# Kernel tuning notes

Measured on AMD Instinct MI355X. Metric: run time of the kernel, lower is better.

The kernel has to match this reference:

```python
import jax, jax.numpy as jnp
import numpy as np

D_MODEL = 2048
N_HEADS = 16
D_K = D_MODEL // N_HEADS


def setup_inputs() -> dict:
    key = jax.random.key(0)
    ks = jax.random.split(key, 11)
    B, S = 2, 2048
    s = 1.0 / np.sqrt(D_MODEL)
    inp = {
        "q": jax.random.normal(ks[0], (B, S, D_MODEL), jnp.float32),
        "k": jax.random.normal(ks[1], (B, S, D_MODEL), jnp.float32),
        "v": jax.random.normal(ks[2], (B, S, D_MODEL), jnp.float32),
        "Wq": jax.random.normal(ks[3], (D_MODEL, D_MODEL), jnp.float32) * s,
        "bq": jnp.zeros((D_MODEL,), jnp.float32),
        "Wk": jax.random.normal(ks[4], (D_MODEL, D_MODEL), jnp.float32) * s,
        "bk": jnp.zeros((D_MODEL,), jnp.float32),
        "Wv": jax.random.normal(ks[5], (D_MODEL, D_MODEL), jnp.float32) * s,
        "bv": jnp.zeros((D_MODEL,), jnp.float32),
        "Wo": jax.random.normal(ks[6], (D_MODEL, D_MODEL), jnp.float32) * s,
        "bo": jnp.zeros((D_MODEL,), jnp.float32),
    }
    return inp


def reference(q, k, v, Wq, bq, Wk, bk, Wv, bv, Wo, bo):
    B, S, _ = q.shape
    # projections, split into heads: [B, H, S, Dk]
    def proj(x, W, b):
        y = jnp.einsum('bsd,de->bse', x, W) + b
        return y.reshape(B, -1, N_HEADS, D_K).transpose(0, 2, 1, 3)
    qh = proj(q, Wq, bq)
    kh = proj(k, Wk, bk)
    vh = proj(v, Wv, bv)
    scores = jnp.einsum('bhqd,bhkd->bhqk', qh, kh) / jnp.sqrt(jnp.float32(D_K))
    attn = jax.nn.softmax(scores, axis=-1)  # dropout is identity in eval mode
    out = jnp.einsum('bhqk,bhkd->bhqd', attn, vh)
    out = out.transpose(0, 2, 1, 3).reshape(B, -1, D_MODEL)
    return jnp.einsum('bsd,de->bse', out, Wo) + bo
```

## Files before the change

### kernel.cpp

```cpp
#include <hip/hip_runtime.h>
#include <math.h>
#include <stdint.h>

constexpr int B_  = 2;
constexpr int S_  = 2048;
constexpr int D_  = 2048;
constexpr int H_  = 16;
constexpr int DK_ = 128;
constexpr int M_  = B_ * S_;

typedef __attribute__((ext_vector_type(8))) _Float16 f16x8;
typedef __attribute__((ext_vector_type(4))) _Float16 f16x4;
typedef __attribute__((ext_vector_type(4))) float    f32x4;

__device__ __forceinline__ void async_copy16(const void* g, void* l) {
    __builtin_amdgcn_global_load_lds(
        (const __attribute__((address_space(1))) unsigned int*)(uintptr_t)g,
        (__attribute__((address_space(3))) unsigned int*)(uintptr_t)l,
        16, 0, 0);
}

__global__ __launch_bounds__(256) void convert_h_rows(const float* __restrict__ X0,
                                                      const float* __restrict__ X1,
                                                      const float* __restrict__ X2,
                                                      _Float16* __restrict__ Y0,
                                                      _Float16* __restrict__ Y1,
                                                      _Float16* __restrict__ Y2) {
    const float* X = blockIdx.z == 0 ? X0 : (blockIdx.z == 1 ? X1 : X2);
    _Float16*   Y  = blockIdx.z == 0 ? Y0 : (blockIdx.z == 1 ? Y1 : Y2);
    const size_t off = ((size_t)blockIdx.x * 256 + threadIdx.x) * 8;
    const float4 a = *reinterpret_cast<const float4*>(X + off);
    const float4 b = *reinterpret_cast<const float4*>(X + off + 4);
    f16x8 y;
    y[0] = (_Float16)a.x; y[1] = (_Float16)a.y; y[2] = (_Float16)a.z; y[3] = (_Float16)a.w;
    y[4] = (_Float16)b.x; y[5] = (_Float16)b.y; y[6] = (_Float16)b.z; y[7] = (_Float16)b.w;
    *reinterpret_cast<f16x8*>(Y + off) = y;
}

__global__ __launch_bounds__(256) void convert_h_T(const float* __restrict__ W0,
                                                   const float* __restrict__ W1,
                                                   const float* __restrict__ W2,
                                                   const float* __restrict__ W3,
                                                   _Float16* __restrict__ Y0,
                                                   _Float16* __restrict__ Y1,
                                                   _Float16* __restrict__ Y2,
                                                   _Float16* __restrict__ Y3) {
    const float* W = blockIdx.z == 0 ? W0 : (blockIdx.z == 1 ? W1 : (blockIdx.z == 2 ? W2 : W3));
    _Float16*   Y  = blockIdx.z == 0 ? Y0 : (blockIdx.z == 1 ? Y1 : (blockIdx.z == 2 ? Y2 : Y3));
    __shared__ float tile[64][65];
    const int k0  = blockIdx.y * 64;
    const int n0  = blockIdx.x * 64;
    const int tid = threadIdx.x;
    const int rr  = tid >> 4;
    const int cc4 = (tid & 15) << 2;
#pragma unroll
    for (int r = 0; r < 4; ++r) {
        const int krow = r * 16 + rr;
        const float4 v = *reinterpret_cast<const float4*>(
            W + (size_t)(k0 + krow) * D_ + n0 + cc4);
        tile[krow][cc4 + 0] = v.x;
        tile[krow][cc4 + 1] = v.y;
        tile[krow][cc4 + 2] = v.z;
        tile[krow][cc4 + 3] = v.w;
    }
    __syncthreads();
#pragma unroll
    for (int r = 0; r < 4; ++r) {
        const int nrow = r * 16 + rr;
        f16x4 y;
        y[0] = (_Float16)tile[cc4 + 0][nrow];
        y[1] = (_Float16)tile[cc4 + 1][nrow];
        y[2] = (_Float16)tile[cc4 + 2][nrow];
        y[3] = (_Float16)tile[cc4 + 3][nrow];
        *reinterpret_cast<f16x4*>(Y + (size_t)(n0 + nrow) * D_ + k0 + cc4) = y;
    }
}

template <int MODE, int COLBLOCKS>
__device__ __forceinline__ void gemm_body(const _Float16* __restrict__ A,
                                          const _Float16* __restrict__ Bt,
                                          const float* __restrict__ bias,
                                          void* __restrict__ Cout,
                                          _Float16* As, _Float16* Bs) {
    const int tid   = threadIdx.x;
    const int wv    = tid >> 6;
    const int lane  = tid & 63;
    const int quad  = lane >> 4;
    const int tq    = lane & 15;
    const int waveM = (wv >> 1) << 6;
    const int waveN = (wv & 1) << 6;

    const int flat    = blockIdx.x;
    const int rowBase = (flat / COLBLOCKS) * 128;
    const int colBase = (flat % COLBLOCKS) * 128;

    const int srow = lane >> 2;
    const int skel = (lane & 3) << 3;

    const _Float16* gA = A + (size_t)(rowBase + wv * 32 + srow) * D_ + skel;
    const _Float16* gB = Bt + (size_t)(colBase + wv * 32 + srow) * D_ + skel;
    _Float16* lA = As + (wv * 32) * 32;
    _Float16* lB = Bs + (wv * 32) * 32;

    f32x4 acc[4][4] = {};

    for (int k0 = 0; k0 < D_; k0 += 32) {
#pragma unroll
        for (int t = 0; t < 2; ++t) {
            async_copy16(gA + (size_t)t * 16 * D_, lA + t * 16 * 32);
            async_copy16(gB + (size_t)t * 16 * D_, lB + t * 16 * 32);
        }
        gA += 32;
        gB += 32;
        __syncthreads();

        f16x8 af[4], bfr[4];
#pragma unroll
        for (int i = 0; i < 4; ++i)
            af[i] = *reinterpret_cast<const f16x8*>(As + (waveM + i * 16 + tq) * 32 + quad * 8);
#pragma unroll
        for (int c = 0; c < 4; ++c)
            bfr[c] = *reinterpret_cast<const f16x8*>(Bs + (waveN + c * 16 + tq) * 32 + quad * 8);
#pragma unroll
        for (int i = 0; i < 4; ++i)
#pragma unroll
            for (int c = 0; c < 4; ++c)
                acc[i][c] = __builtin_amdgcn_mfma_f32_16x16x32_f16(bfr[c], af[i], acc[i][c], 0, 0, 0);
        __syncthreads();
    }

#pragma unroll
    for (int i = 0; i < 4; ++i) {
        const int m = rowBase + waveM + i * 16 + tq;
#pragma unroll
        for (int c = 0; c < 4; ++c) {
            const int n0 = colBase + waveN + c * 16 + (quad << 2);
            if (MODE == 0) {
                const float4 b4 = *reinterpret_cast<const float4*>(&bias[n0]);
                float4 o;
                o.x = acc[i][c][0] + b4.x;
                o.y = acc[i][c][1] + b4.y;
                o.z = acc[i][c][2] + b4.z;
                o.w = acc[i][c][3] + b4.w;
                *reinterpret_cast<float4*>(&((float*)Cout)[(size_t)m * D_ + n0]) = o;
            } else if (MODE == 1) {
                const float4 b4 = *reinterpret_cast<const float4*>(&bias[n0]);
                f16x4 y;
                y[0] = (_Float16)(acc[i][c][0] + b4.x);
                y[1] = (_Float16)(acc[i][c][1] + b4.y);
                y[2] = (_Float16)(acc[i][c][2] + b4.z);
                y[3] = (_Float16)(acc[i][c][3] + b4.w);
                const int b = m >> 11, s = m & 2047;
                const int h = n0 >> 7, d0 = n0 & 127;
                *reinterpret_cast<f16x4*>(
                    &((_Float16*)Cout)[(((size_t)(b * H_ + h) * S_) + s) * DK_ + d0]) = y;
            } else {
                const float bvr = bias[m];
                f16x4 y;
                y[0] = (_Float16)(acc[i][c][0] + bvr);
                y[1] = (_Float16)(acc[i][c][1] + bvr);
                y[2] = (_Float16)(acc[i][c][2] + bvr);
                y[3] = (_Float16)(acc[i][c][3] + bvr);
                const int h = m >> 7, dd = m & 127;
                const int b = n0 >> 11, s0 = n0 & 2047;
                *reinterpret_cast<f16x4*>(
                    &((_Float16*)Cout)[(((size_t)(b * H_ + h) * DK_) + dd) * S_ + s0]) = y;
            }
        }
    }
}

__global__ __launch_bounds__(256) void gemm_qkv(const _Float16* Aq, const _Float16* Wq, const float* bq, _Float16* Qo,
                                                const _Float16* Ak, const _Float16* Wk, const float* bk, _Float16* Ko,
                                                const _Float16* Wv, const _Float16* Av, const float* bv, _Float16* Vo) {
    __shared__ _Float16 As[128 * 32];
    __shared__ _Float16 Bs[128 * 32];
    if (blockIdx.z == 0)       gemm_body<1, 16>(Aq, Wq, bq, Qo, As, Bs);
    else if (blockIdx.z == 1)  gemm_body<1, 16>(Ak, Wk, bk, Ko, As, Bs);
    else                       gemm_body<2, 32>(Wv, Av, bv, Vo, As, Bs);
}

__global__ __launch_bounds__(256) void gemm_wo(const _Float16* A, const _Float16* Wt,
                                               const float* bias, float* Out) {
    __shared__ _Float16 As[128 * 32];
    __shared__ _Float16 Bs[128 * 32];
    gemm_body<0, 16>(A, Wt, bias, Out, As, Bs);
}

__global__ __launch_bounds__(256, 2) void attn_mfma(const _Float16* __restrict__ Qb,
                                                    const _Float16* __restrict__ Kb,
                                                    const _Float16* __restrict__ Vtb,
                                                    _Float16* __restrict__ Af) {
    __shared__ _Float16 Ks[128 * 128];
    __shared__ _Float16 Vts[128 * 128];

    const int tid  = threadIdx.x;
    const int wv   = tid >> 6;
    const int lane = tid & 63;
    const int quad = lane >> 4;
    const int tq   = lane & 15;

    const int bh = blockIdx.y;
    const int b  = bh >> 4;
    const int h  = bh & 15;
    const int q0 = blockIdx.x * 128 + wv * 32;

    const _Float16* Qw  = Qb + ((size_t)bh * S_ + q0) * DK_;
    const _Float16* Kbh = Kb + (size_t)bh * S_ * DK_;
    const _Float16* Vbh = Vtb + (size_t)bh * DK_ * S_;

    f16x8 qf[2][4];
#pragma unroll
    for (int i = 0; i < 2; ++i)
#pragma unroll
        for (int kd = 0; kd < 4; ++kd)
            qf[i][kd] = *reinterpret_cast<const f16x8*>(
                Qw + (size_t)(i * 16 + tq) * DK_ + kd * 32 + quad * 8);

    f32x4 ofrag[2][8] = {};
    float l_i[2] = {0.f, 0.f};
    const float scale = 0.08838834764831845f;
    const float SHIFT = 8.0f;

    for (int kt = 0; kt < S_; kt += 128) {
        __syncthreads();
#pragma unroll
        for (int c = 0; c < 8; ++c) {
            const int r0  = wv * 32 + c * 4;
            const int row = r0 + (lane >> 4);
            const int cg  = (lane & 15) ^ (row & 7);
            async_copy16(Kbh + (size_t)(kt + row) * DK_ + cg * 8, Ks + r0 * 128);
        }
#pragma unroll
        for (int c = 0; c < 8; ++c) {
            const int d0 = wv * 32 + c * 4;
            const int d  = d0 + (lane >> 4);
            const int cg = (lane & 15) ^ (d & 7);
            async_copy16(Vbh + (size_t)d * S_ + kt + cg * 8, Vts + d0 * 128);
        }
        __syncthreads();

        f32x4 st[8][2] = {};
#pragma unroll
        for (int kd = 0; kd < 4; ++kd) {
            const int ch = (kd * 4 + quad) ^ (tq & 7);
#pragma unroll
            for (int kk = 0; kk < 8; ++kk) {
                const f16x8 kf = *reinterpret_cast<const f16x8*>(
                    Ks + (kk * 16 + tq) * 128 + ch * 8);
#pragma unroll
                for (int i = 0; i < 2; ++i)
                    st[kk][i] = __builtin_amdgcn_mfma_f32_16x16x32_f16(kf, qf[i][kd], st[kk][i], 0, 0, 0);
            }
        }

        unsigned int w[2][8][2];
#pragma unroll
        for (int i = 0; i < 2; ++i) {
            float sum = 0.f;
#pragma unroll
            for (int kk = 0; kk < 8; ++kk) {
                float p[4];
#pragma unroll
                for (int r = 0; r < 4; ++r) {
                    p[r] = __expf(st[kk][i][r] * scale - SHIFT);
                    sum += p[r];
                }
#pragma unroll
                for (int m2 = 0; m2 < 2; ++m2) {
                    union { _Float16 hh[2]; unsigned int u; } pk;
                    pk.hh[0] = (_Float16)p[2 * m2];
                    pk.hh[1] = (_Float16)p[2 * m2 + 1];
                    w[i][kk][m2] = pk.u;
                }
            }
            l_i[i] += sum;
        }

#pragma unroll
        for (int ks = 0; ks < 4; ++ks) {
            f16x8 pf[2];
#pragma unroll
            for (int i = 0; i < 2; ++i) {
                union { unsigned int u[4]; f16x8 v; } pu;
#pragma unroll
                for (int u = 0; u < 4; ++u) {
                    const int src = tq + 16 * (2 * (quad & 1) + (u >> 1));
                    const int va = __shfl((int)w[i][2 * ks + 0][u & 1], src, 64);
                    const int vb = __shfl((int)w[i][2 * ks + 1][u & 1], src, 64);
                    pu.u[u] = (quad >= 2) ? (unsigned int)vb : (unsigned int)va;
                }
                pf[i] = pu.v;
            }
            const int ch = (ks * 4 + quad) ^ (tq & 7);
#pragma unroll
            for (int dt = 0; dt < 8; ++dt) {
                const f16x8 vf = *reinterpret_cast<const f16x8*>(
                    Vts + (dt * 16 + tq) * 128 + ch * 8);
#pragma unroll
                for (int i = 0; i < 2; ++i)
                    ofrag[i][dt] = __builtin_amdgcn_mfma_f32_16x16x32_f16(pf[i], vf, ofrag[i][dt], 0, 0, 0);
            }
        }
    }

#pragma unroll
    for (int i = 0; i < 2; ++i) {
        l_i[i] += __shfl_xor(l_i[i], 16, 64);
        l_i[i] += __shfl_xor(l_i[i], 32, 64);
    }

#pragma unroll
    for (int i = 0; i < 2; ++i) {
        const float invl_own = 1.0f / l_i[i];
#pragma unroll
        for (int r = 0; r < 4; ++r) {
            const float invl = __shfl(invl_own, quad * 4 + r, 64);
            const int srow = q0 + i * 16 + quad * 4 + r;
            _Float16* arow = Af + ((size_t)(b * S_ + srow)) * D_ + h * DK_;
#pragma unroll
            for (int dt = 0; dt < 8; ++dt)
                arow[dt * 16 + tq] = (_Float16)(ofrag[i][dt][r] * invl);
        }
    }
}

extern "C" void kernel_launch(void* const* d_in, const int* in_sizes, int n_in,
                              void* d_out, int out_size, void* d_ws, size_t ws_size,
                              hipStream_t stream) {
    const float* q  = (const float*)d_in[0];
    const float* k  = (const float*)d_in[1];
    const float* v  = (const float*)d_in[2];
    const float* Wq = (const float*)d_in[3];
    const float* bq = (const float*)d_in[4];
    const float* Wk = (const float*)d_in[5];
    const float* bk = (const float*)d_in[6];
    const float* Wv = (const float*)d_in[7];
    const float* bv = (const float*)d_in[8];
    const float* Wo = (const float*)d_in[9];
    const float* bo = (const float*)d_in[10];
    float* out = (float*)d_out;

    const size_t mat  = (size_t)M_ * D_;
    const size_t wmat = (size_t)D_ * D_;

    _Float16* A2q = (_Float16*)d_ws;
    _Float16* A2k = A2q + mat;
    _Float16* A2v = A2k + mat;
    _Float16* W2q = A2v + mat;
    _Float16* W2k = W2q + wmat;
    _Float16* W2v = W2k + wmat;
    _Float16* W2o = W2v + wmat;
    _Float16* Qb  = W2o + wmat;
    _Float16* Kb  = Qb + mat;
    _Float16* Vtb = Kb + mat;
    _Float16* Af  = A2q;

    convert_h_rows<<<dim3((unsigned)(mat / 8 / 256), 1, 3), 256, 0, stream>>>(
        q, k, v, A2q, A2k, A2v);
    convert_h_T<<<dim3(32, 32, 4), 256, 0, stream>>>(Wq, Wk, Wv, Wo, W2q, W2k, W2v, W2o);

    gemm_qkv<<<dim3(512, 1, 3), 256, 0, stream>>>(A2q, W2q, bq, Qb,
                                                  A2k, W2k, bk, Kb,
                                                  W2v, A2v, bv, Vtb);

    attn_mfma<<<dim3(S_ / 128, B_ * H_), 256, 0, stream>>>(Qb, Kb, Vtb, Af);

    gemm_wo<<<dim3(512), 256, 0, stream>>>(Af, W2o, bo, out);
}
```

Measured before the change: 468.1 us.

## Use 32x32x16 MFMA with XOR-swizzled LDS in GEMMs; merge conversion kernels

The GEMM body moves from 16x16x32 MFMA tiles to 32x32x16 MFMA tiles, with 2x2 accumulators of 16 floats per wave. The LDS staging now uses an XOR swizzle on the 8-element k-chunks, and the fragment reads and epilogue indexing are updated to match. The goal is fewer MFMA issues, fewer LDS reads per FLOP, and fewer bank conflicts. The two fp32-to-fp16 conversion kernels are also merged into a single launch, which saves one kernel launch.

```diff
diff --git a/kernel.cpp b/kernel.cpp
--- a/kernel.cpp
+++ b/kernel.cpp
@@ -9,9 +9,10 @@
 constexpr int DK_ = 128;
 constexpr int M_  = B_ * S_;
 
-typedef __attribute__((ext_vector_type(8))) _Float16 f16x8;
-typedef __attribute__((ext_vector_type(4))) _Float16 f16x4;
-typedef __attribute__((ext_vector_type(4))) float    f32x4;
+typedef __attribute__((ext_vector_type(8)))  _Float16 f16x8;
+typedef __attribute__((ext_vector_type(4)))  _Float16 f16x4;
+typedef __attribute__((ext_vector_type(4)))  float    f32x4;
+typedef __attribute__((ext_vector_type(16))) float    f32x16;
 
 __device__ __forceinline__ void async_copy16(const void* g, void* l) {
     __builtin_amdgcn_global_load_lds(
@@ -20,59 +21,65 @@
         16, 0, 0);
 }
 
-__global__ __launch_bounds__(256) void convert_h_rows(const float* __restrict__ X0,
-                                                      const float* __restrict__ X1,
-                                                      const float* __restrict__ X2,
-                                                      _Float16* __restrict__ Y0,
-                                                      _Float16* __restrict__ Y1,
-                                                      _Float16* __restrict__ Y2) {
-    const float* X = blockIdx.z == 0 ? X0 : (blockIdx.z == 1 ? X1 : X2);
-    _Float16*   Y  = blockIdx.z == 0 ? Y0 : (blockIdx.z == 1 ? Y1 : Y2);
-    const size_t off = ((size_t)blockIdx.x * 256 + threadIdx.x) * 8;
-    const float4 a = *reinterpret_cast<const float4*>(X + off);
-    const float4 b = *reinterpret_cast<const float4*>(X + off + 4);
-    f16x8 y;
-    y[0] = (_Float16)a.x; y[1] = (_Float16)a.y; y[2] = (_Float16)a.z; y[3] = (_Float16)a.w;
-    y[4] = (_Float16)b.x; y[5] = (_Float16)b.y; y[6] = (_Float16)b.z; y[7] = (_Float16)b.w;
-    *reinterpret_cast<f16x8*>(Y + off) = y;
-}
-
-__global__ __launch_bounds__(256) void convert_h_T(const float* __restrict__ W0,
-                                                   const float* __restrict__ W1,
-                                                   const float* __restrict__ W2,
-                                                   const float* __restrict__ W3,
-                                                   _Float16* __restrict__ Y0,
-                                                   _Float16* __restrict__ Y1,
-                                                   _Float16* __restrict__ Y2,
-                                                   _Float16* __restrict__ Y3) {
-    const float* W = blockIdx.z == 0 ? W0 : (blockIdx.z == 1 ? W1 : (blockIdx.z == 2 ? W2 : W3));
-    _Float16*   Y  = blockIdx.z == 0 ? Y0 : (blockIdx.z == 1 ? Y1 : (blockIdx.z == 2 ? Y2 : Y3));
-    __shared__ float tile[64][65];
-    const int k0  = blockIdx.y * 64;
-    const int n0  = blockIdx.x * 64;
+__global__ __launch_bounds__(256) void convert_all(const float* __restrict__ q,
+                                                   const float* __restrict__ k,
+                                                   const float* __restrict__ v,
+                                                   const float* __restrict__ Wq,
+                                                   const float* __restrict__ Wk,
+                                                   const float* __restrict__ Wv,
+                                                   const float* __restrict__ Wo,
+                                                   _Float16* __restrict__ Yq,
+                                                   _Float16* __restrict__ Yk,
+                                                   _Float16* __restrict__ Yv,
+                                                   _Float16* __restrict__ YWq,
+                                                   _Float16* __restrict__ YWk,
+                                                   _Float16* __restrict__ YWv,
+                                                   _Float16* __restrict__ YWo) {
+    const int z   = blockIdx.z;
     const int tid = threadIdx.x;
-    const int rr  = tid >> 4;
-    const int cc4 = (tid & 15) << 2;
-#pragma unroll
-    for (int r = 0; r < 4; ++r) {
-        const int krow = r * 16 + rr;
-        const float4 v = *reinterpret_cast<const float4*>(
-            W + (size_t)(k0 + krow) * D_ + n0 + cc4);
-        tile[krow][cc4 + 0] = v.x;
-        tile[krow][cc4 + 1] = v.y;
-        tile[krow][cc4 + 2] = v.z;
-        tile[krow][cc4 + 3] = v.w;
-    }
-    __syncthreads();
-#pragma unroll
-    for (int r = 0; r < 4; ++r) {
-        const int nrow = r * 16 + rr;
-        f16x4 y;
-        y[0] = (_Float16)tile[cc4 + 0][nrow];
-        y[1] = (_Float16)tile[cc4 + 1][nrow];
-        y[2] = (_Float16)tile[cc4 + 2][nrow];
-        y[3] = (_Float16)tile[cc4 + 3][nrow];
-        *reinterpret_cast<f16x4*>(Y + (size_t)(n0 + nrow) * D_ + k0 + cc4) = y;
+    if (z < 3) {
+        const float* X = z == 0 ? q : (z == 1 ? k : v);
+        _Float16*   Y  = z == 0 ? Yq : (z == 1 ? Yk : Yv);
+        const int flat = blockIdx.y * 32 + blockIdx.x;
+#pragma unroll
+        for (int it = 0; it < 4; ++it) {
+            const size_t off = (((size_t)(flat + it * 1024)) * 256 + tid) * 8;
+            const float4 a = *reinterpret_cast<const float4*>(X + off);
+            const float4 b = *reinterpret_cast<const float4*>(X + off + 4);
+            f16x8 y;
+            y[0] = (_Float16)a.x; y[1] = (_Float16)a.y; y[2] = (_Float16)a.z; y[3] = (_Float16)a.w;
+            y[4] = (_Float16)b.x; y[5] = (_Float16)b.y; y[6] = (_Float16)b.z; y[7] = (_Float16)b.w;
+            *reinterpret_cast<f16x8*>(Y + off) = y;
+        }
+    } else {
+        const float* W = z == 3 ? Wq : (z == 4 ? Wk : (z == 5 ? Wv : Wo));
+        _Float16*   Y  = z == 3 ? YWq : (z == 4 ? YWk : (z == 5 ? YWv : YWo));
+        __shared__ float tile[64][65];
+        const int k0  = blockIdx.y * 64;
+        const int n0  = blockIdx.x * 64;
+        const int rr  = tid >> 4;
+        const int cc4 = (tid & 15) << 2;
+#pragma unroll
+        for (int r = 0; r < 4; ++r) {
+            const int krow = r * 16 + rr;
+            const float4 w4 = *reinterpret_cast<const float4*>(
+                W + (size_t)(k0 + krow) * D_ + n0 + cc4);
+            tile[krow][cc4 + 0] = w4.x;
+            tile[krow][cc4 + 1] = w4.y;
+            tile[krow][cc4 + 2] = w4.z;
+            tile[krow][cc4 + 3] = w4.w;
+        }
+        __syncthreads();
+#pragma unroll
+        for (int r = 0; r < 4; ++r) {
+            const int nrow = r * 16 + rr;
+            f16x4 y;
+            y[0] = (_Float16)tile[cc4 + 0][nrow];
+            y[1] = (_Float16)tile[cc4 + 1][nrow];
+            y[2] = (_Float16)tile[cc4 + 2][nrow];
+            y[3] = (_Float16)tile[cc4 + 3][nrow];
+            *reinterpret_cast<f16x4*>(Y + (size_t)(n0 + nrow) * D_ + k0 + cc4) = y;
+        }
     }
 }
 
@@ -85,8 +92,8 @@
     const int tid   = threadIdx.x;
     const int wv    = tid >> 6;
     const int lane  = tid & 63;
-    const int quad  = lane >> 4;
-    const int tq    = lane & 15;
+    const int l31   = lane & 31;
+    const int lh    = lane >> 5;
     const int waveM = (wv >> 1) << 6;
     const int waveN = (wv & 1) << 6;
 
@@ -95,14 +102,14 @@
     const int colBase = (flat % COLBLOCKS) * 128;
 
     const int srow = lane >> 2;
-    const int skel = (lane & 3) << 3;
+    const int skel = (((lane & 3) ^ (srow & 3)) << 3);
 
     const _Float16* gA = A + (size_t)(rowBase + wv * 32 + srow) * D_ + skel;
     const _Float16* gB = Bt + (size_t)(colBase + wv * 32 + srow) * D_ + skel;
     _Float16* lA = As + (wv * 32) * 32;
     _Float16* lB = Bs + (wv * 32) * 32;
 
-    f32x4 acc[4][4] = {};
+    f32x16 acc[2][2] = {};
 
     for (int k0 = 0; k0 < D_; k0 += 32) {
 #pragma unroll
@@ -114,57 +121,66 @@
         gB += 32;
         __syncthreads();
 
-        f16x8 af[4], bfr[4];
-#pragma unroll
-        for (int i = 0; i < 4; ++i)
-            af[i] = *reinterpret_cast<const f16x8*>(As + (waveM + i * 16 + tq) * 32 + quad * 8);
-#pragma unroll
-        for (int c = 0; c < 4; ++c)
-            bfr[c] = *reinterpret_cast<const f16x8*>(Bs + (waveN + c * 16 + tq) * 32 + quad * 8);
-#pragma unroll
-        for (int i = 0; i < 4; ++i)
-#pragma unroll
-            for (int c = 0; c < 4; ++c)
-                acc[i][c] = __builtin_amdgcn_mfma_f32_16x16x32_f16(bfr[c], af[i], acc[i][c], 0, 0, 0);
-        __syncthreads();
-    }
-
-#pragma unroll
-    for (int i = 0; i < 4; ++i) {
-        const int m = rowBase + waveM + i * 16 + tq;
-#pragma unroll
-        for (int c = 0; c < 4; ++c) {
-            const int n0 = colBase + waveN + c * 16 + (quad << 2);
-            if (MODE == 0) {
-                const float4 b4 = *reinterpret_cast<const float4*>(&bias[n0]);
-                float4 o;
-                o.x = acc[i][c][0] + b4.x;
-                o.y = acc[i][c][1] + b4.y;
-                o.z = acc[i][c][2] + b4.z;
-                o.w = acc[i][c][3] + b4.w;
-                *reinterpret_cast<float4*>(&((float*)Cout)[(size_t)m * D_ + n0]) = o;
-            } else if (MODE == 1) {
-                const float4 b4 = *reinterpret_cast<const float4*>(&bias[n0]);
-                f16x4 y;
-                y[0] = (_Float16)(acc[i][c][0] + b4.x);
-                y[1] = (_Float16)(acc[i][c][1] + b4.y);
-                y[2] = (_Float16)(acc[i][c][2] + b4.z);
-                y[3] = (_Float16)(acc[i][c][3] + b4.w);
-                const int b = m >> 11, s = m & 2047;
-                const int h = n0 >> 7, d0 = n0 & 127;
-                *reinterpret_cast<f16x4*>(
-                    &((_Float16*)Cout)[(((size_t)(b * H_ + h) * S_) + s) * DK_ + d0]) = y;
-            } else {
-                const float bvr = bias[m];
-                f16x4 y;
-                y[0] = (_Float16)(acc[i][c][0] + bvr);
-                y[1] = (_Float16)(acc[i][c][1] + bvr);
-                y[2] = (_Float16)(acc[i][c][2] + bvr);
-                y[3] = (_Float16)(acc[i][c][3] + bvr);
-                const int h = m >> 7, dd = m & 127;
-                const int b = n0 >> 11, s0 = n0 & 2047;
-                *reinterpret_cast<f16x4*>(
-                    &((_Float16*)Cout)[(((size_t)(b * H_ + h) * DK_) + dd) * S_ + s0]) = y;
+        const int x3 = lane & 3;
+#pragma unroll
+        for (int ks = 0; ks < 2; ++ks) {
+            const int ch = ((ks * 2 + lh) ^ x3) << 3;
+            f16x8 af[2], bfr[2];
+#pragma unroll
+            for (int c = 0; c < 2; ++c) {
+                af[c]  = *reinterpret_cast<const f16x8*>(As + (waveM + c * 32 + l31) * 32 + ch);
+                bfr[c] = *reinterpret_cast<const f16x8*>(Bs + (waveN + c * 32 + l31) * 32 + ch);
+            }
+#pragma unroll
+            for (int cm = 0; cm < 2; ++cm)
+#pragma unroll
+                for (int cn = 0; cn < 2; ++cn)
+                    acc[cm][cn] = __builtin_amdgcn_mfma_f32_32x32x16_f16(
+                        bfr[cn], af[cm], acc[cm][cn], 0, 0, 0);
+        }
+        __syncthreads();
+    }
+
+#pragma unroll
+    for (int cm = 0; cm < 2; ++cm) {
+        const int m = rowBase + waveM + cm * 32 + l31;
+#pragma unroll
+        for (int cn = 0; cn < 2; ++cn) {
+#pragma unroll
+            for (int g = 0; g < 4; ++g) {
+                const int n0 = colBase + waveN + cn * 32 + 8 * g + 4 * lh;
+                const float v0 = acc[cm][cn][g * 4 + 0];
+                const float v1 = acc[cm][cn][g * 4 + 1];
+                const float v2 = acc[cm][cn][g * 4 + 2];
+                const float v3 = acc[cm][cn][g * 4 + 3];
+                if (MODE == 0) {
+                    const float4 b4 = *reinterpret_cast<const float4*>(&bias[n0]);
+                    float4 o;
+                    o.x = v0 + b4.x; o.y = v1 + b4.y; o.z = v2 + b4.z; o.w = v3 + b4.w;
+                    *reinterpret_cast<float4*>(&((float*)Cout)[(size_t)m * D_ + n0]) = o;
+                } else if (MODE == 1) {
+                    const float4 b4 = *reinterpret_cast<const float4*>(&bias[n0]);
+                    f16x4 y;
+                    y[0] = (_Float16)(v0 + b4.x);
+                    y[1] = (_Float16)(v1 + b4.y);
+                    y[2] = (_Float16)(v2 + b4.z);
+                    y[3] = (_Float16)(v3 + b4.w);
+                    const int b = m >> 11, s = m & 2047;
+                    const int h = n0 >> 7, d0 = n0 & 127;
+                    *reinterpret_cast<f16x4*>(
+                        &((_Float16*)Cout)[(((size_t)(b * H_ + h) * S_) + s) * DK_ + d0]) = y;
+                } else {
+                    const float bvr = bias[m];
+                    f16x4 y;
+                    y[0] = (_Float16)(v0 + bvr);
+                    y[1] = (_Float16)(v1 + bvr);
+                    y[2] = (_Float16)(v2 + bvr);
+                    y[3] = (_Float16)(v3 + bvr);
+                    const int h = m >> 7, dd = m & 127;
+                    const int b = n0 >> 11, s0 = n0 & 2047;
+                    *reinterpret_cast<f16x4*>(
+                        &((_Float16*)Cout)[(((size_t)(b * H_ + h) * DK_) + dd) * S_ + s0]) = y;
+                }
             }
         }
     }
@@ -356,9 +372,8 @@
     _Float16* Vtb = Kb + mat;
     _Float16* Af  = A2q;
 
-    convert_h_rows<<<dim3((unsigned)(mat / 8 / 256), 1, 3), 256, 0, stream>>>(
-        q, k, v, A2q, A2k, A2v);
-    convert_h_T<<<dim3(32, 32, 4), 256, 0, stream>>>(Wq, Wk, Wv, Wo, W2q, W2k, W2v, W2o);
+    convert_all<<<dim3(32, 32, 7), 256, 0, stream>>>(q, k, v, Wq, Wk, Wv, Wo,
+                                                     A2q, A2k, A2v, W2q, W2k, W2v, W2o);
 
     gemm_qkv<<<dim3(512, 1, 3), 256, 0, stream>>>(A2q, W2q, bq, Qb,
                                                   A2k, W2k, bk, Kb,
```

New measurement: 507.8 us. 1.08x slower.
